# Kernel optimization log

Hardware: AMD Instinct MI355X
Metric: run time of the kernel (lower is better)

The kernel has to match this reference:

```python
import jax, jax.numpy as jnp
from jax import lax
import numpy as np

B, DIM, HF, H, W, P = 4, 64, 128, 256, 256, 8  # patch_size = 8


def setup_inputs() -> dict:
    key = jax.random.key(0)
    k0, k1, k2, k3, k4 = jax.random.split(key, 5)
    C2 = 2 * HF
    x = jax.random.normal(k0, (B, DIM, H, W), dtype=jnp.float32)
    w_in = jax.random.normal(k1, (C2, DIM), dtype=jnp.float32) * 0.05      # 1x1 conv weight
    w_dw = jax.random.normal(k2, (C2, 1, 3, 3), dtype=jnp.float32) * 0.1   # depthwise 3x3
    fft_filt = 1.0 + 0.1 * jax.random.normal(k3, (C2, 1, 1, P, P // 2 + 1), dtype=jnp.float32)
    w_out = jax.random.normal(k4, (DIM, HF), dtype=jnp.float32) * 0.05     # 1x1 conv weight
    return {"x": x, "w_in": w_in, "w_dw": w_dw, "fft_filt": fft_filt, "w_out": w_out}


def reference(x, w_in, w_dw, fft_filt, w_out):
    # project_in: 1x1 conv (no bias)
    h = jnp.einsum('oc,bchw->bohw', w_in, x)
    b, c, hh, ww = h.shape
    # b c (h p1) (w p2) -> b c h w p1 p2
    hp = h.reshape(b, c, hh // P, P, ww // P, P).transpose(0, 1, 2, 4, 3, 5)
    # patchwise spectral gating
    f = jnp.fft.rfft2(hp.astype(jnp.float32)) * fft_filt
    hp = jnp.fft.irfft2(f, s=(P, P))
    # b c h w p1 p2 -> b c (h p1) (w p2)
    h = hp.transpose(0, 1, 2, 4, 3, 5).reshape(b, c, hh, ww)
    # depthwise 3x3 conv, SAME padding, groups = channels
    h = lax.conv_general_dilated(h, w_dw, (1, 1), 'SAME',
                                 feature_group_count=c,
                                 dimension_numbers=('NCHW', 'OIHW', 'NCHW'))
    x1, x2 = jnp.split(h, 2, axis=1)
    g = jax.nn.gelu(x1, approximate=False) * x2
    # project_out: 1x1 conv
    return jnp.einsum('oc,bchw->bohw', w_out, g)
```

## Files before the change

### kernel.cpp

```cpp
#include <hip/hip_runtime.h>
#include <hip/hip_bf16.h>

#define NB 4
#define DIMC 64
#define C2 256
#define HFC 128
#define HH 256
#define WW 256
#define HW (HH * WW)

typedef __attribute__((ext_vector_type(8))) short short8;
typedef __attribute__((ext_vector_type(4))) float f32x4;

__device__ __forceinline__ f32x4 mfma16(short8 a, short8 b, f32x4 c) {
  return __builtin_amdgcn_mfma_f32_16x16x32_bf16(a, b, c, 0, 0, 0);
}

__device__ __forceinline__ short f2bs(float f) {
  __hip_bfloat16 h = __float2bfloat16(f);
  union { __hip_bfloat16 h; short s; } u; u.h = h;
  return u.s;
}

__device__ __forceinline__ float bs2f(short s) {
  union { float f; unsigned u; } v;
  v.u = ((unsigned)(unsigned short)s) << 16;
  return v.f;
}

__device__ __forceinline__ float fast_gelu(float u) {
  float au = fabsf(u);
  float z = au * 0.70710678118654752f;
  float e = __expf(-z * z);
  float t = __builtin_amdgcn_rcpf(fmaf(0.3275911f, z, 1.0f));
  float p = fmaf(t, 1.061405429f, -1.453152027f);
  p = fmaf(t, p, 1.421413741f);
  p = fmaf(t, p, -0.284496736f);
  p = fmaf(t, p, 0.254829592f);
  p *= t;
  return fmaxf(u, 0.f) - 0.5f * au * p * e;
}

__global__ __launch_bounds__(64) void prep_kernel(
    const float* __restrict__ w_in, const float* __restrict__ fft,
    const float* __restrict__ w_out, __hip_bfloat16* __restrict__ A1,
    __hip_bfloat16* __restrict__ A2, __hip_bfloat16* __restrict__ Mf) {
  int blk = blockIdx.x;
  int l = threadIdx.x;
  int mm = l & 15, qj = l >> 4;
  if (blk < C2) {
    __shared__ float Feff[64];
    __shared__ float kc[64];
    __shared__ float ct[8];
    if (l < 8) {
      const float s = 0.70710678118654752f;
      const float v0[8] = {1.f, s, 0.f, -s, -1.f, -s, 0.f, s};
      ct[l] = v0[l];
    }
    int c = blk;
    const float* f = fft + c * 40;
    int u = l >> 3, v = l & 7;
    int um = (8 - u) & 7;
    float val;
    if (v <= 4) {
      val = f[u * 5 + v];
      if (v == 0 || v == 4) val = 0.5f * (val + f[um * 5 + v]);
    } else {
      val = f[um * 5 + (8 - v)];
    }
    Feff[l] = val;
    __syncthreads();
    int dy = l >> 3, dx = l & 7;
    float s = 0.f;
    for (int uu = 0; uu < 8; ++uu)
      for (int vv = 0; vv < 8; ++vv)
        s += Feff[uu * 8 + vv] * ct[(uu * dy + vv * dx) & 7];
    kc[l] = s * (1.f / 64.f);
    __syncthreads();
    for (int mb = 0; mb < 4; ++mb) {
      int p = mb * 16 + mm;
      int py = p >> 3, px = p & 7;
      for (int kb = 0; kb < 2; ++kb)
        for (int j = 0; j < 8; ++j) {
          int q = kb * 32 + qj * 8 + j;
          int qy = q >> 3, qx = q & 7;
          float kv = kc[((py - qy) & 7) * 8 + ((px - qx) & 7)];
          Mf[(size_t)c * 4096 + (size_t)((mb * 2 + kb) * 64 + l) * 8 + j] =
              __float2bfloat16(kv);
        }
    }
  } else if (blk == C2) {
    for (int mb = 0; mb < 16; ++mb)
      for (int kb = 0; kb < 2; ++kb)
        for (int j = 0; j < 8; ++j) {
          int m = mb * 16 + mm, k = kb * 32 + qj * 8 + j;
          A1[(size_t)((mb * 2 + kb) * 64 + l) * 8 + j] =
              __float2bfloat16(w_in[m * 64 + k]);
        }
  } else {
    for (int mb = 0; mb < 4; ++mb)
      for (int kb = 0; kb < 4; ++kb)
        for (int j = 0; j < 8; ++j) {
          int m = mb * 16 + mm, k = kb * 32 + qj * 8 + j;
          A2[(size_t)((mb * 4 + kb) * 64 + l) * 8 + j] =
              __float2bfloat16(w_out[m * 128 + k]);
        }
  }
}

#define FS_LDS_BYTES 81920

__device__ __forceinline__ int hs_idx(int cL, int row, int patch, int qx) {
  int p2 = patch ^ ((cL >> 2) << 1) ^ row;
  return 32768 + cL * 512 + row * 64 + p2 * 8 + qx;
}

__global__ __launch_bounds__(256, 2) void fs_kernel(
    const float* __restrict__ x, const __hip_bfloat16* __restrict__ A1,
    const __hip_bfloat16* __restrict__ Mf, __hip_bfloat16* __restrict__ h) {
  extern __shared__ char smem[];
  short* lds = reinterpret_cast<short*>(smem);
  int pg = blockIdx.x, b = blockIdx.y;
  int Py = pg >> 2, x0 = (pg & 3) * 64;
  int t = threadIdx.x;
  int w = t >> 6, l = t & 63;
  int g = l >> 4;
  int nn16 = l & 15;

  {
    int n = t & 63, dgrp = t >> 6;
    int nblk = n >> 4, nn = n & 15;
#pragma unroll
    for (int py = 0; py < 8; ++py) {
      const float* xb =
          x + (size_t)b * DIMC * HW + (size_t)(Py * 8 + py) * WW + x0 + n;
#pragma unroll
      for (int s = 0; s < 2; ++s) {
        int jb = dgrp + s * 4;
        int kb = jb >> 2, quad = jb & 3;
        short8 pk;
#pragma unroll
        for (int j = 0; j < 8; ++j) pk[j] = f2bs(xb[(size_t)(jb * 8 + j) * HW]);
        *reinterpret_cast<short8*>(
            &lds[(size_t)(py * 512 + (kb * 4 + nblk) * 64 + quad * 16 + nn) * 8]) = pk;
      }
    }
  }
  __syncthreads();

  const short8* A1v = reinterpret_cast<const short8*>(A1);
  const short8* Mfv = reinterpret_cast<const short8*>(Mf);
  const short8* xv = reinterpret_cast<const short8*>(lds);

  for (int i = 0; i < 16; ++i) {
    short8 af0 = A1v[(i * 2 + 0) * 64 + l];
    short8 af1 = A1v[(i * 2 + 1) * 64 + l];
#pragma unroll
    for (int py2 = 0; py2 < 2; ++py2) {
      int py = w * 2 + py2;
#pragma unroll
      for (int nb = 0; nb < 4; ++nb) {
        short8 b0 = xv[py * 512 + (0 * 4 + nb) * 64 + l];
        short8 b1 = xv[py * 512 + (1 * 4 + nb) * 64 + l];
        f32x4 acc = (f32x4){0.f, 0.f, 0.f, 0.f};
        acc = mfma16(af0, b0, acc);
        acc = mfma16(af1, b1, acc);
        int xc = nb * 16 + nn16;
#pragma unroll
        for (int r = 0; r < 4; ++r) {
          int cL = g * 4 + r;
          lds[hs_idx(cL, py, xc >> 3, xc & 7)] = f2bs(acc[r]);
        }
      }
    }
    __syncthreads();

    int p8 = l & 7;
#pragma unroll
    for (int k = 0; k < 4; ++k) {
      int cL = w * 4 + k;
      int c = i * 16 + cL;
      short8 mf[8];
#pragma unroll
      for (int mb = 0; mb < 4; ++mb)
#pragma unroll
        for (int kb = 0; kb < 2; ++kb)
          mf[mb * 2 + kb] = Mfv[(size_t)c * 512 + (mb * 2 + kb) * 64 + l];
      short8 bs0 = *reinterpret_cast<const short8*>(&lds[hs_idx(cL, g, p8, 0)]);
      short8 bs1 = *reinterpret_cast<const short8*>(&lds[hs_idx(cL, 4 + g, p8, 0)]);
      f32x4 accs[4];
#pragma unroll
      for (int mb = 0; mb < 4; ++mb) {
        accs[mb] = (f32x4){0.f, 0.f, 0.f, 0.f};
        accs[mb] = mfma16(mf[mb * 2 + 0], bs0, accs[mb]);
        accs[mb] = mfma16(mf[mb * 2 + 1], bs1, accs[mb]);
      }
      if (nn16 < 8) {
        __hip_bfloat16* ob = h + ((size_t)(b * C2 + c)) * HW +
                             (size_t)(Py * 8) * WW + x0 + nn16 * 8;
#pragma unroll
        for (int mb = 0; mb < 4; ++mb)
#pragma unroll
          for (int r = 0; r < 4; ++r) {
            int p = mb * 16 + g * 4 + r;
            ob[(p >> 3) * WW + (p & 7)] = __float2bfloat16(accs[mb][r]);
          }
      }
    }
    __syncthreads();
  }
}

__global__ __launch_bounds__(256) void dwgelu_kernel(
    const __hip_bfloat16* __restrict__ h2, const float* __restrict__ w_dw,
    __hip_bfloat16* __restrict__ gf) {
  __shared__ short ldsJ[8 * 1024];
  int jb = blockIdx.x;
  int y0 = blockIdx.y * 4;
  int b = blockIdx.z;
  int t = threadIdx.x;
  int j = t >> 5, xg = t & 31;
  int x0 = xg * 8;
  int c1 = jb * 8 + j, c2 = c1 + HFC;
  const __hip_bfloat16* hbase = h2 + (size_t)b * C2 * HW;

  float wd1[9], wd2[9];
#pragma unroll
  for (int k = 0; k < 9; ++k) {
    wd1[k] = w_dw[c1 * 9 + k];
    wd2[k] = w_dw[c2 * 9 + k];
  }

  float acc1[4][8], acc2[4][8];
#pragma unroll
  for (int r = 0; r < 4; ++r)
#pragma unroll
    for (int i = 0; i < 8; ++i) { acc1[r][i] = 0.f; acc2[r][i] = 0.f; }

#pragma unroll
  for (int ir = -1; ir <= 4; ++ir) {
    int yy = y0 + ir;
    bool valid = (yy >= 0) && (yy < HH);
    float f1[10], f2[10];
    if (valid) {
      const __hip_bfloat16* r1 = hbase + ((size_t)c1 * HH + yy) * WW;
      const __hip_bfloat16* r2 = hbase + ((size_t)c2 * HH + yy) * WW;
      short8 v1 = *reinterpret_cast<const short8*>(r1 + x0);
      short8 v2 = *reinterpret_cast<const short8*>(r2 + x0);
#pragma unroll
      for (int i = 0; i < 8; ++i) { f1[i + 1] = bs2f(v1[i]); f2[i + 1] = bs2f(v2[i]); }
      f1[0] = (x0 > 0) ? __bfloat162float(r1[x0 - 1]) : 0.f;
      f2[0] = (x0 > 0) ? __bfloat162float(r2[x0 - 1]) : 0.f;
      f1[9] = (x0 + 8 < WW) ? __bfloat162float(r1[x0 + 8]) : 0.f;
      f2[9] = (x0 + 8 < WW) ? __bfloat162float(r2[x0 + 8]) : 0.f;
    } else {
#pragma unroll
      for (int i = 0; i < 10; ++i) { f1[i] = 0.f; f2[i] = 0.f; }
    }
#pragma unroll
    for (int dy = -1; dy <= 1; ++dy) {
      int r = ir - dy;
      if (r < 0 || r >= 4) continue;
      int ky = dy + 1;
#pragma unroll
      for (int i = 0; i < 8; ++i) {
        acc1[r][i] += f1[i] * wd1[ky * 3] + f1[i + 1] * wd1[ky * 3 + 1] +
                      f1[i + 2] * wd1[ky * 3 + 2];
        acc2[r][i] += f2[i] * wd2[ky * 3] + f2[i + 1] * wd2[ky * 3 + 1] +
                      f2[i + 2] * wd2[ky * 3 + 2];
      }
    }
  }

#pragma unroll
  for (int r = 0; r < 4; ++r) {
    short8 pk;
#pragma unroll
    for (int i = 0; i < 8; ++i) {
      float gg = fast_gelu(acc1[r][i]);
      pk[i] = f2bs(gg * acc2[r][i]);
    }
    *reinterpret_cast<short8*>(&ldsJ[j * 1024 + r * 256 + x0]) = pk;
  }
  __syncthreads();

  int kb = jb >> 2, quad = jb & 3;
  short8* gfv = reinterpret_cast<short8*>(gf) + (size_t)b * 1048576;
#pragma unroll
  for (int k = 0; k < 4; ++k) {
    short8 v;
#pragma unroll
    for (int j2 = 0; j2 < 8; ++j2) v[j2] = ldsJ[j2 * 1024 + k * 256 + t];
    int pix = (y0 + k) * WW + t;
    gfv[((size_t)(pix >> 4) * 4 + kb) * 64 + quad * 16 + (pix & 15)] = v;
  }
}

__global__ __launch_bounds__(256) void gemm2_kernel(
    const __hip_bfloat16* __restrict__ gf, const __hip_bfloat16* __restrict__ A2,
    float* __restrict__ out) {
  int b = blockIdx.y;
  int pix0 = blockIdx.x * 256;
  int tid = threadIdx.x;
  int w = tid >> 6, l = tid & 63;
  int quad = l >> 4, ln = l & 15;
  const short8* A2v = reinterpret_cast<const short8*>(A2);
  short8 af[4][4];
#pragma unroll
  for (int mb = 0; mb < 4; ++mb)
#pragma unroll
    for (int kb = 0; kb < 4; ++kb) af[mb][kb] = A2v[(mb * 4 + kb) * 64 + l];
  const short8* gv = reinterpret_cast<const short8*>(gf) + (size_t)b * 1048576;
  f32x4 acc[4][4];
#pragma unroll
  for (int i = 0; i < 4; ++i)
#pragma unroll
    for (int j = 0; j < 4; ++j) acc[i][j] = (f32x4){0.f, 0.f, 0.f, 0.f};
#pragma unroll
  for (int nb = 0; nb < 4; ++nb) {
    size_t pixblk = (size_t)blockIdx.x * 16 + w * 4 + nb;
    short8 bf[4];
#pragma unroll
    for (int kb = 0; kb < 4; ++kb) bf[kb] = gv[(pixblk * 4 + kb) * 64 + l];
#pragma unroll
    for (int mb = 0; mb < 4; ++mb)
#pragma unroll
      for (int kb = 0; kb < 4; ++kb)
        acc[mb][nb] = mfma16(af[mb][kb], bf[kb], acc[mb][nb]);
  }
#pragma unroll
  for (int mb = 0; mb < 4; ++mb)
#pragma unroll
    for (int nb = 0; nb < 4; ++nb)
#pragma unroll
      for (int r = 0; r < 4; ++r) {
        int o = mb * 16 + quad * 4 + r;
        int pix = pix0 + w * 64 + nb * 16 + ln;
        out[((size_t)b * DIMC + o) * HW + pix] = acc[mb][nb][r];
      }
}

extern "C" void kernel_launch(void* const* d_in, const int* in_sizes, int n_in,
                              void* d_out, int out_size, void* d_ws,
                              size_t ws_size, hipStream_t stream) {
  const float* x = (const float*)d_in[0];
  const float* w_in = (const float*)d_in[1];
  const float* w_dw = (const float*)d_in[2];
  const float* fft = (const float*)d_in[3];
  const float* w_out = (const float*)d_in[4];
  float* out = (float*)d_out;
  char* ws = (char*)d_ws;
  __hip_bfloat16* A1 = (__hip_bfloat16*)(ws);
  __hip_bfloat16* A2 = (__hip_bfloat16*)(ws + 32768);
  __hip_bfloat16* Mf = (__hip_bfloat16*)(ws + 49152);
  __hip_bfloat16* gf = (__hip_bfloat16*)(ws + 2146304);
  __hip_bfloat16* h = (__hip_bfloat16*)(ws + 69255168);

  static bool fs_attr_set = false;
  if (!fs_attr_set) {
    (void)hipFuncSetAttribute((const void*)fs_kernel,
                              hipFuncAttributeMaxDynamicSharedMemorySize,
                              FS_LDS_BYTES);
    fs_attr_set = true;
  }

  prep_kernel<<<258, 64, 0, stream>>>(w_in, fft, w_out, A1, A2, Mf);
  fs_kernel<<<dim3(128, NB), 256, FS_LDS_BYTES, stream>>>(x, A1, Mf, h);
  dwgelu_kernel<<<dim3(16, 64, NB), 256, 0, stream>>>(h, w_dw, gf);
  gemm2_kernel<<<dim3(256, NB), 256, 0, stream>>>(gf, A2, out);
}
```

Measured before the change: 313.6 us.

## Prefetch spectral and projection weights and stage outputs through LDS for vector stores

Software-pipelines the global loads of the per-channel spectral matrices and the project-in weights, using double-buffered registers so each next load is issued before the current MFMA work. The spectral output is also staged in a per-channel LDS slot, then written back as one 16-byte vector store per lane. This replaces the earlier scattered 2-byte global stores. The aims are to hide global load latency and to coalesce the writes of h, at the cost of more registers, which matters under the 2-blocks occupancy bound. The staging also reuses the spectral input region of LDS, which relies on lgkmcnt waits within a wave.

```diff
diff --git a/kernel.cpp b/kernel.cpp
--- a/kernel.cpp
+++ b/kernel.cpp
@@ -115,6 +115,42 @@
   return 32768 + cL * 512 + row * 64 + p2 * 8 + qx;
 }
 
+__device__ __forceinline__ void load_mf(short8* dst, const short8* Mfv, int c,
+                                        int l) {
+#pragma unroll
+  for (int f = 0; f < 8; ++f) dst[f] = Mfv[(size_t)c * 512 + f * 64 + l];
+}
+
+__device__ __forceinline__ void spec_one(short* lds, const short8* mf, int cL,
+                                         int cg, int g, int nn16, int l,
+                                         __hip_bfloat16* hb, int Py, int x0) {
+  int p8 = l & 7;
+  short8 bs0 = *reinterpret_cast<const short8*>(&lds[hs_idx(cL, g, p8, 0)]);
+  short8 bs1 = *reinterpret_cast<const short8*>(&lds[hs_idx(cL, 4 + g, p8, 0)]);
+  f32x4 accs[4];
+#pragma unroll
+  for (int mb = 0; mb < 4; ++mb) {
+    accs[mb] = (f32x4){0.f, 0.f, 0.f, 0.f};
+    accs[mb] = mfma16(mf[mb * 2 + 0], bs0, accs[mb]);
+    accs[mb] = mfma16(mf[mb * 2 + 1], bs1, accs[mb]);
+  }
+  int slot = 32768 + cL * 512;
+  if (nn16 < 8) {
+#pragma unroll
+    for (int mb = 0; mb < 4; ++mb)
+#pragma unroll
+      for (int r = 0; r < 4; ++r) {
+        int p = mb * 16 + g * 4 + r;
+        lds[slot + (p >> 3) * 64 + nn16 * 8 + (p & 7)] = f2bs(accs[mb][r]);
+      }
+  }
+  asm volatile("s_waitcnt lgkmcnt(0)" ::: "memory");
+  short8 ov = *reinterpret_cast<const short8*>(&lds[slot + l * 8]);
+  __hip_bfloat16* hp = hb + (size_t)cg * HW +
+                       (size_t)(Py * 8 + (l >> 3)) * WW + x0 + (l & 7) * 8;
+  *reinterpret_cast<short8*>(hp) = ov;
+}
+
 __global__ __launch_bounds__(256, 2) void fs_kernel(
     const float* __restrict__ x, const __hip_bfloat16* __restrict__ A1,
     const __hip_bfloat16* __restrict__ Mf, __hip_bfloat16* __restrict__ h) {
@@ -127,6 +163,15 @@
   int g = l >> 4;
   int nn16 = l & 15;
 
+  const short8* A1v = reinterpret_cast<const short8*>(A1);
+  const short8* Mfv = reinterpret_cast<const short8*>(Mf);
+  __hip_bfloat16* hb = h + (size_t)b * C2 * HW;
+
+  short8 afA0 = A1v[0 * 64 + l];
+  short8 afA1 = A1v[1 * 64 + l];
+  short8 mfA[8], mfB[8];
+  load_mf(mfA, Mfv, w * 4, l);
+
   {
     int n = t & 63, dgrp = t >> 6;
     int nblk = n >> 4, nn = n & 15;
@@ -148,13 +193,9 @@
   }
   __syncthreads();
 
-  const short8* A1v = reinterpret_cast<const short8*>(A1);
-  const short8* Mfv = reinterpret_cast<const short8*>(Mf);
   const short8* xv = reinterpret_cast<const short8*>(lds);
 
   for (int i = 0; i < 16; ++i) {
-    short8 af0 = A1v[(i * 2 + 0) * 64 + l];
-    short8 af1 = A1v[(i * 2 + 1) * 64 + l];
 #pragma unroll
     for (int py2 = 0; py2 < 2; ++py2) {
       int py = w * 2 + py2;
@@ -163,8 +204,8 @@
         short8 b0 = xv[py * 512 + (0 * 4 + nb) * 64 + l];
         short8 b1 = xv[py * 512 + (1 * 4 + nb) * 64 + l];
         f32x4 acc = (f32x4){0.f, 0.f, 0.f, 0.f};
-        acc = mfma16(af0, b0, acc);
-        acc = mfma16(af1, b1, acc);
+        acc = mfma16(afA0, b0, acc);
+        acc = mfma16(afA1, b1, acc);
         int xc = nb * 16 + nn16;
 #pragma unroll
         for (int r = 0; r < 4; ++r) {
@@ -173,41 +214,24 @@
         }
       }
     }
+    int inx = (i + 1) & 15;
+    short8 afN0 = A1v[(inx * 2 + 0) * 64 + l];
+    short8 afN1 = A1v[(inx * 2 + 1) * 64 + l];
     __syncthreads();
 
-    int p8 = l & 7;
-#pragma unroll
-    for (int k = 0; k < 4; ++k) {
-      int cL = w * 4 + k;
-      int c = i * 16 + cL;
-      short8 mf[8];
-#pragma unroll
-      for (int mb = 0; mb < 4; ++mb)
-#pragma unroll
-        for (int kb = 0; kb < 2; ++kb)
-          mf[mb * 2 + kb] = Mfv[(size_t)c * 512 + (mb * 2 + kb) * 64 + l];
-      short8 bs0 = *reinterpret_cast<const short8*>(&lds[hs_idx(cL, g, p8, 0)]);
-      short8 bs1 = *reinterpret_cast<const short8*>(&lds[hs_idx(cL, 4 + g, p8, 0)]);
-      f32x4 accs[4];
-#pragma unroll
-      for (int mb = 0; mb < 4; ++mb) {
-        accs[mb] = (f32x4){0.f, 0.f, 0.f, 0.f};
-        accs[mb] = mfma16(mf[mb * 2 + 0], bs0, accs[mb]);
-        accs[mb] = mfma16(mf[mb * 2 + 1], bs1, accs[mb]);
-      }
-      if (nn16 < 8) {
-        __hip_bfloat16* ob = h + ((size_t)(b * C2 + c)) * HW +
-                             (size_t)(Py * 8) * WW + x0 + nn16 * 8;
-#pragma unroll
-        for (int mb = 0; mb < 4; ++mb)
-#pragma unroll
-          for (int r = 0; r < 4; ++r) {
-            int p = mb * 16 + g * 4 + r;
-            ob[(p >> 3) * WW + (p & 7)] = __float2bfloat16(accs[mb][r]);
-          }
-      }
-    }
+    int c0 = i * 16 + w * 4;
+    load_mf(mfB, Mfv, c0 + 1, l);
+    spec_one(lds, mfA, w * 4 + 0, c0 + 0, g, nn16, l, hb, Py, x0);
+    load_mf(mfA, Mfv, c0 + 2, l);
+    spec_one(lds, mfB, w * 4 + 1, c0 + 1, g, nn16, l, hb, Py, x0);
+    load_mf(mfB, Mfv, c0 + 3, l);
+    spec_one(lds, mfA, w * 4 + 2, c0 + 2, g, nn16, l, hb, Py, x0);
+    load_mf(mfA, Mfv, inx * 16 + w * 4, l);
+    spec_one(lds, mfB, w * 4 + 3, c0 + 3, g, nn16, l, hb, Py, x0);
     __syncthreads();
+
+    afA0 = afN0;
+    afA1 = afN1;
   }
 }
 
```

New measurement: 260.3 us. 17.0% less time.
